# Performance work log

Measured on AMD Instinct MI355X. Metric: run time of the kernel, lower is better.

Reference implementation:

```python
import jax, jax.numpy as jnp
import numpy as np

S_GRID = 14.0
L_COORD = 5.0
L_NOOBJ = 0.5
B = 2


def _xywh2xyxy(b):
    # b: [..., 4] with (x, y, w, h); x,y are divided by S per the original module
    xy = b[..., :2] / S_GRID
    wh = b[..., 2:4]
    return jnp.concatenate([xy - 0.5 * wh, xy + 0.5 * wh], axis=-1)


def setup_inputs() -> dict:
    key = jax.random.key(0)
    k1, k2, k3, k4 = jax.random.split(key, 4)
    N, S, C = 4096, 14, 20
    pred_tensor = jax.random.uniform(k1, (N, S, S, B * 5 + C), dtype=jnp.float32, minval=0.05, maxval=1.0)
    target_boxes = jax.random.uniform(k2, (N, S, S, 4), dtype=jnp.float32, minval=0.05, maxval=1.0)
    target_cls = jax.random.normal(k3, (N, S, S, C), dtype=jnp.float32)
    has_object_map = jax.random.randint(k4, (N, S, S), 0, 2).astype(jnp.bool_)
    return {"pred_tensor": pred_tensor, "target_boxes": target_boxes,
            "target_cls": target_cls, "has_object_map": has_object_map}


def reference(pred_tensor, target_boxes, target_cls, has_object_map):
    N = pred_tensor.shape[0]
    mask = has_object_map                      # [N,S,S] bool
    maskf = mask.astype(pred_tensor.dtype)
    pb = pred_tensor[..., :B * 5].reshape(*pred_tensor.shape[:3], B, 5)  # [N,S,S,B,5]
    pc = pred_tensor[..., B * 5:]              # [N,S,S,20]

    # class loss: masked sum of squared errors over classes
    cls_loss = jnp.sum(maskf * jnp.sum((target_cls - pc) ** 2, axis=-1))

    # no-object loss: conf^2 on cells without objects, summed over both boxes
    conf = pb[..., 4]                          # [N,S,S,B]
    no_obj_loss = L_NOOBJ * jnp.sum(jnp.where(~mask[..., None], conf, 0.0) ** 2)

    # per-cell IoU of target vs each of the B predicted boxes (diag of original NxM)
    t_xyxy = _xywh2xyxy(target_boxes)          # [N,S,S,4]
    p_xyxy = _xywh2xyxy(pb[..., :4])           # [N,S,S,B,4]
    lt = jnp.maximum(t_xyxy[..., None, :2], p_xyxy[..., :2])
    rb = jnp.minimum(t_xyxy[..., None, 2:], p_xyxy[..., 2:])
    wh = jnp.clip(rb - lt, 0.0)
    inter = wh[..., 0] * wh[..., 1]            # [N,S,S,B]
    area_t = (t_xyxy[..., 2] - t_xyxy[..., 0]) * (t_xyxy[..., 3] - t_xyxy[..., 1])
    area_p = (p_xyxy[..., 2] - p_xyxy[..., 0]) * (p_xyxy[..., 3] - p_xyxy[..., 1])
    iou = inter / (area_t[..., None] + area_p - inter)  # [N,S,S,B]

    best_iou = jnp.max(iou, axis=-1)           # [N,S,S]
    best_idx = jnp.argmax(iou, axis=-1)        # [N,S,S]
    best_box = jnp.take_along_axis(pb, best_idx[..., None, None], axis=3)[..., 0, :]  # [N,S,S,5]

    xy_diff = jnp.where(mask[..., None], best_box[..., :2] - target_boxes[..., :2], 0.0)
    wh_p = jnp.where(mask[..., None], best_box[..., 2:4], 1.0)
    wh_t = jnp.where(mask[..., None], target_boxes[..., 2:4], 1.0)
    reg_loss = L_COORD * (jnp.sum(xy_diff ** 2)
                          + jnp.sum((jnp.sqrt(wh_p) - jnp.sqrt(wh_t)) ** 2))

    # containing-object confidence loss: mse(best_iou, best_box_conf) on object cells
    containing_obj_loss = jnp.sum(jnp.where(mask, best_iou - best_box[..., 4], 0.0) ** 2)

    total_loss = (cls_loss + no_obj_loss + reg_loss + containing_obj_loss) / N
    return (total_loss, reg_loss, containing_obj_loss, no_obj_loss, cls_loss)
```

## Files before the change

kernel.cpp:

```cpp
#include <hip/hip_runtime.h>
#include <math.h>


#define BLOCK 256
#define WPB 4
#define CPW 64

__global__ __launch_bounds__(BLOCK, 8) void k_yolo(
    const float*  __restrict__ pred,
    const float4* __restrict__ tbox4,
    const float2* __restrict__ tcls2,
    const int*    __restrict__ mask,
    float4*       __restrict__ partial,
    int n_cells)
{
    __shared__ float2 sbox[WPB][CPW * 5];
    const int tid  = threadIdx.x;
    const int lane = tid & 63;
    const int w    = tid >> 6;
    const long long cell0 = ((long long)blockIdx.x * WPB + w) * CPW;

    long long rem = (long long)n_cells - cell0;
    int lim = rem < 0 ? 0 : (rem > CPW ? CPW : (int)rem);

    float cls = 0.f, noobj = 0.f, reg = 0.f, cont = 0.f;

    int mflag = 0;
    float4 tb = make_float4(0.f, 0.f, 0.f, 0.f);
    if (lane < lim) {
        mflag = mask[cell0 + lane];
        tb    = tbox4[cell0 + lane];
    }

    const float2* p2  = reinterpret_cast<const float2*>(pred) + cell0 * 15;
    const float2* t2  = tcls2 + cell0 * 10;
    float2*       sb2 = sbox[w];

    #pragma unroll
    for (int k = 0; k < 15; ++k) {
        int j = lane + (k << 6);
        int c = j / 15;
        int r = j - c * 15;
        int mc = __shfl(mflag, c, 64);
        if (c < lim) {
            float2 v = p2[j];
            if (r < 5) {
                sb2[c * 5 + r] = v;
            } else if (mc) {
                float2 t = t2[c * 10 + (r - 5)];
                float d0 = t.x - v.x, d1 = t.y - v.y;
                cls = fmaf(d0, d0, cls);
                cls = fmaf(d1, d1, cls);
            }
        }
    }

    asm volatile("s_waitcnt lgkmcnt(0)" ::: "memory");
    __builtin_amdgcn_sched_barrier(0);

    if (lane < lim) {
        const float2* bl = sb2 + lane * 5;
        float2 v0 = bl[0], v1 = bl[1], v2 = bl[2], v3 = bl[3], v4 = bl[4];
        if (mflag) {
            float txc = tb.x / 14.0f, tyc = tb.y / 14.0f;
            float t0 = txc - 0.5f * tb.z, t1 = tyc - 0.5f * tb.w;
            float t2c = txc + 0.5f * tb.z, t3 = tyc + 0.5f * tb.w;
            float area_t = (t2c - t0) * (t3 - t1);
            float bx[2] = { v0.x, v2.y }, by[2] = { v0.y, v3.x };
            float bw[2] = { v1.x, v3.y }, bh[2] = { v1.y, v4.x };
            float bcf[2] = { v2.x, v4.y };
            float iou[2];
            #pragma unroll
            for (int b = 0; b < 2; ++b) {
                float px = bx[b] / 14.0f, py = by[b] / 14.0f;
                float q0 = px - 0.5f * bw[b], q1 = py - 0.5f * bh[b];
                float q2 = px + 0.5f * bw[b], q3 = py + 0.5f * bh[b];
                float lt0 = fmaxf(t0, q0), lt1 = fmaxf(t1, q1);
                float rb0 = fminf(t2c, q2), rb1 = fminf(t3, q3);
                float ww = fmaxf(rb0 - lt0, 0.f), hh = fmaxf(rb1 - lt1, 0.f);
                float inter = ww * hh;
                float area_p = (q2 - q0) * (q3 - q1);
                iou[b] = inter / (area_t + area_p - inter);
            }
            int bi = (iou[1] > iou[0]) ? 1 : 0;
            float dx = bx[bi] - tb.x, dy = by[bi] - tb.y;
            float swd = sqrtf(bw[bi]) - sqrtf(tb.z);
            float shd = sqrtf(bh[bi]) - sqrtf(tb.w);
            reg = 5.0f * (dx*dx + dy*dy + swd*swd + shd*shd);
            float dco = iou[bi] - bcf[bi];
            cont = dco * dco;
        } else {
            noobj = 0.5f * (v2.x * v2.x + v4.y * v4.y);
        }
    }

    #pragma unroll
    for (int off = 32; off; off >>= 1) {
        cls   += __shfl_down(cls,   off, 64);
        noobj += __shfl_down(noobj, off, 64);
        reg   += __shfl_down(reg,   off, 64);
        cont  += __shfl_down(cont,  off, 64);
    }
    __shared__ float4 swr[WPB];
    if (lane == 0) swr[w] = make_float4(cls, noobj, reg, cont);
    __syncthreads();
    if (tid == 0) {
        float4 a = swr[0];
        #pragma unroll
        for (int i = 1; i < WPB; ++i) {
            float4 b = swr[i];
            a.x += b.x; a.y += b.y; a.z += b.z; a.w += b.w;
        }
        partial[blockIdx.x] = a;
    }
}

__global__ __launch_bounds__(BLOCK) void k_final(
    const float4* __restrict__ partial, int nblocks,
    float* __restrict__ out, float invN)
{
    float4 acc = make_float4(0.f, 0.f, 0.f, 0.f);
    for (int b = threadIdx.x; b < nblocks; b += BLOCK) {
        float4 v = partial[b];
        acc.x += v.x; acc.y += v.y; acc.z += v.z; acc.w += v.w;
    }
    #pragma unroll
    for (int off = 32; off; off >>= 1) {
        acc.x += __shfl_down(acc.x, off, 64);
        acc.y += __shfl_down(acc.y, off, 64);
        acc.z += __shfl_down(acc.z, off, 64);
        acc.w += __shfl_down(acc.w, off, 64);
    }
    __shared__ float4 sw[WPB];
    int lane = threadIdx.x & 63, w = threadIdx.x >> 6;
    if (lane == 0) sw[w] = acc;
    __syncthreads();
    if (threadIdx.x == 0) {
        float cls = 0.f, noobj = 0.f, reg = 0.f, cont = 0.f;
        #pragma unroll
        for (int i = 0; i < WPB; ++i) {
            cls += sw[i].x; noobj += sw[i].y; reg += sw[i].z; cont += sw[i].w;
        }
        out[0] = (cls + noobj + reg + cont) * invN;
        out[1] = reg;
        out[2] = cont;
        out[3] = noobj;
        out[4] = cls;
    }
}

extern "C" void kernel_launch(void* const* d_in, const int* in_sizes, int n_in,
                              void* d_out, int out_size, void* d_ws, size_t ws_size,
                              hipStream_t stream) {
    const float*  pred  = (const float*)d_in[0];
    const float4* tbox4 = (const float4*)d_in[1];
    const float2* tcls2 = (const float2*)d_in[2];
    const int*    mask  = (const int*)d_in[3];
    float* out = (float*)d_out;
    float4* partial = (float4*)d_ws;

    int n_cells = in_sizes[3];
    int N = in_sizes[0] / (14 * 14 * 30);
    int nblocks = (n_cells + BLOCK - 1) / BLOCK;

    hipLaunchKernelGGL(k_yolo, dim3(nblocks), dim3(BLOCK), 0, stream,
                       pred, tbox4, tcls2, mask, partial, n_cells);
    hipLaunchKernelGGL(k_final, dim3(1), dim3(BLOCK), 0, stream,
                       partial, nblocks, out, 1.0f / (float)N);
}
```

Before: 207.3 us.

## Stage whole pred rows into LDS via global_load_lds and vectorize class loads

Each wave now copies its 64 cells of pred (30 floats each) straight from global memory into LDS with async global_load_lds 16-byte transfers, replacing the strided float2 gather loop with its divide-by-15 indexing. Each object-cell lane then reads its own target class row as five float4 loads and computes the class loss from LDS. This removes per-element index arithmetic and shuffles and widens the loads. The cost is a much larger LDS footprint (lower occupancy hint of 5), per-lane uncoalesced 80-byte tcls reads, and LDS bank conflicts from the 30-float row stride.

Result: faster. 200.2 us (-3.4%).

```diff
diff --git a/kernel.cpp b/kernel.cpp
--- a/kernel.cpp
+++ b/kernel.cpp
@@ -6,15 +6,15 @@
 #define WPB 4
 #define CPW 64
 
-__global__ __launch_bounds__(BLOCK, 8) void k_yolo(
+__global__ __launch_bounds__(BLOCK, 5) void k_yolo(
     const float*  __restrict__ pred,
     const float4* __restrict__ tbox4,
-    const float2* __restrict__ tcls2,
+    const float4* __restrict__ tcls4,
     const int*    __restrict__ mask,
     float4*       __restrict__ partial,
     int n_cells)
 {
-    __shared__ float2 sbox[WPB][CPW * 5];
+    __shared__ float sp[WPB][CPW * 30];
     const int tid  = threadIdx.x;
     const int lane = tid & 63;
     const int w    = tid >> 6;
@@ -32,35 +32,42 @@
         tb    = tbox4[cell0 + lane];
     }
 
-    const float2* p2  = reinterpret_cast<const float2*>(pred) + cell0 * 15;
-    const float2* t2  = tcls2 + cell0 * 10;
-    float2*       sb2 = sbox[w];
-
-    #pragma unroll
-    for (int k = 0; k < 15; ++k) {
-        int j = lane + (k << 6);
-        int c = j / 15;
-        int r = j - c * 15;
-        int mc = __shfl(mflag, c, 64);
-        if (c < lim) {
-            float2 v = p2[j];
-            if (r < 5) {
-                sb2[c * 5 + r] = v;
-            } else if (mc) {
-                float2 t = t2[c * 10 + (r - 5)];
-                float d0 = t.x - v.x, d1 = t.y - v.y;
-                cls = fmaf(d0, d0, cls);
-                cls = fmaf(d1, d1, cls);
-            }
+    if (lim == CPW) {
+        const __attribute__((address_space(1))) float4* gp =
+            (const __attribute__((address_space(1))) float4*)(pred + cell0 * 30);
+        __attribute__((address_space(3))) float4* lp =
+            (__attribute__((address_space(3))) float4*)(&sp[w][0]);
+        #pragma unroll
+        for (int i = 0; i < 7; ++i) {
+            __builtin_amdgcn_global_load_lds(
+                (const __attribute__((address_space(1))) void*)(gp + lane + i * 64),
+                (__attribute__((address_space(3))) void*)(lp + i * 64),
+                16, 0, 0);
         }
+        if (lane < 32) {
+            __builtin_amdgcn_global_load_lds(
+                (const __attribute__((address_space(1))) void*)(gp + 448 + lane),
+                (__attribute__((address_space(3))) void*)(lp + 448),
+                16, 0, 0);
+        }
+    } else if (lim > 0) {
+        const float* gsrc = pred + cell0 * 30;
+        for (int k = lane; k < lim * 30; k += 64) sp[w][k] = gsrc[k];
     }
 
-    asm volatile("s_waitcnt lgkmcnt(0)" ::: "memory");
+    float4 tc[5];
+    if (mflag) {
+        const float4* t4 = tcls4 + (cell0 + lane) * 5;
+        #pragma unroll
+        for (int q = 0; q < 5; ++q) tc[q] = t4[q];
+    }
+
+    asm volatile("s_waitcnt vmcnt(0) lgkmcnt(0)" ::: "memory");
     __builtin_amdgcn_sched_barrier(0);
 
     if (lane < lim) {
-        const float2* bl = sb2 + lane * 5;
-        float2 v0 = bl[0], v1 = bl[1], v2 = bl[2], v3 = bl[3], v4 = bl[4];
+        const float2* pc2 = reinterpret_cast<const float2*>(sp[w] + lane * 30);
+        float2 v0 = pc2[0], v1 = pc2[1], v2 = pc2[2], v3 = pc2[3], v4 = pc2[4];
         if (mflag) {
             float txc = tb.x / 14.0f, tyc = tb.y / 14.0f;
             float t0 = txc - 0.5f * tb.z, t1 = tyc - 0.5f * tb.w;
@@ -89,6 +96,18 @@
             reg = 5.0f * (dx*dx + dy*dy + swd*swd + shd*shd);
             float dco = iou[bi] - bcf[bi];
             cont = dco * dco;
+
+            #pragma unroll
+            for (int q = 0; q < 5; ++q) {
+                float2 a = pc2[5 + 2 * q];
+                float2 b = pc2[6 + 2 * q];
+                float d0 = tc[q].x - a.x, d1 = tc[q].y - a.y;
+                float d2 = tc[q].z - b.x, d3 = tc[q].w - b.y;
+                cls = fmaf(d0, d0, cls);
+                cls = fmaf(d1, d1, cls);
+                cls = fmaf(d2, d2, cls);
+                cls = fmaf(d3, d3, cls);
+            }
         } else {
             noobj = 0.5f * (v2.x * v2.x + v4.y * v4.y);
         }
@@ -154,7 +173,7 @@
                               hipStream_t stream) {
     const float*  pred  = (const float*)d_in[0];
     const float4* tbox4 = (const float4*)d_in[1];
-    const float2* tcls2 = (const float2*)d_in[2];
+    const float4* tcls4 = (const float4*)d_in[2];
     const int*    mask  = (const int*)d_in[3];
     float* out = (float*)d_out;
     float4* partial = (float4*)d_ws;
@@ -164,7 +183,7 @@
     int nblocks = (n_cells + BLOCK - 1) / BLOCK;
 
     hipLaunchKernelGGL(k_yolo, dim3(nblocks), dim3(BLOCK), 0, stream,
-                       pred, tbox4, tcls2, mask, partial, n_cells);
+                       pred, tbox4, tcls4, mask, partial, n_cells);
     hipLaunchKernelGGL(k_final, dim3(1), dim3(BLOCK), 0, stream,
                        partial, nblocks, out, 1.0f / (float)N);
 }
```

## Replace LDS-staged coalesced loads with per-thread direct cell loads

Applied to the files above, without the earlier changes.

The kernel stops staging prediction data through shared memory with wave-cooperative coalesced float2 loads and a cross-lane mask shuffle. Each thread now loads its own cell's 30 prediction floats and 20 target-class floats (as float4) straight into registers and computes all loss terms locally. This removes the LDS traffic, the shuffles and the index arithmetic, but the global loads become strided per thread (120-byte stride), which can hurt coalescing. Class targets are loaded even for cells without objects. Register pressure also rises, and the launch-bounds occupancy hint drops from 8 to 6.

After: 203.6 us. Within noise of the previous version (-1.8%).

```diff
diff --git a/kernel.cpp b/kernel.cpp
--- a/kernel.cpp
+++ b/kernel.cpp
@@ -4,63 +4,32 @@
 
 #define BLOCK 256
 #define WPB 4
-#define CPW 64
 
-__global__ __launch_bounds__(BLOCK, 8) void k_yolo(
+__global__ __launch_bounds__(BLOCK, 6) void k_yolo(
     const float*  __restrict__ pred,
     const float4* __restrict__ tbox4,
-    const float2* __restrict__ tcls2,
+    const float4* __restrict__ tcls4,
     const int*    __restrict__ mask,
     float4*       __restrict__ partial,
     int n_cells)
 {
-    __shared__ float2 sbox[WPB][CPW * 5];
     const int tid  = threadIdx.x;
-    const int lane = tid & 63;
-    const int w    = tid >> 6;
-    const long long cell0 = ((long long)blockIdx.x * WPB + w) * CPW;
-
-    long long rem = (long long)n_cells - cell0;
-    int lim = rem < 0 ? 0 : (rem > CPW ? CPW : (int)rem);
+    const int cell = blockIdx.x * BLOCK + tid;
+    const bool valid = cell < n_cells;
 
     float cls = 0.f, noobj = 0.f, reg = 0.f, cont = 0.f;
 
-    int mflag = 0;
-    float4 tb = make_float4(0.f, 0.f, 0.f, 0.f);
-    if (lane < lim) {
-        mflag = mask[cell0 + lane];
-        tb    = tbox4[cell0 + lane];
-    }
+    if (valid) {
+        const float2* pc2 = reinterpret_cast<const float2*>(pred + (size_t)cell * 30);
+        const float4* t4  = tcls4 + (size_t)cell * 5;
 
-    const float2* p2  = reinterpret_cast<const float2*>(pred) + cell0 * 15;
-    const float2* t2  = tcls2 + cell0 * 10;
-    float2*       sb2 = sbox[w];
+        const int    mflag = mask[cell];
+        const float4 tb    = tbox4[cell];
+        float2 v0  = pc2[0],  v1  = pc2[1],  v2  = pc2[2],  v3  = pc2[3],  v4  = pc2[4];
+        float2 v5  = pc2[5],  v6  = pc2[6],  v7  = pc2[7],  v8  = pc2[8],  v9  = pc2[9];
+        float2 v10 = pc2[10], v11 = pc2[11], v12 = pc2[12], v13 = pc2[13], v14 = pc2[14];
+        float4 tc0 = t4[0], tc1 = t4[1], tc2 = t4[2], tc3 = t4[3], tc4 = t4[4];
 
-    #pragma unroll
-    for (int k = 0; k < 15; ++k) {
-        int j = lane + (k << 6);
-        int c = j / 15;
-        int r = j - c * 15;
-        int mc = __shfl(mflag, c, 64);
-        if (c < lim) {
-            float2 v = p2[j];
-            if (r < 5) {
-                sb2[c * 5 + r] = v;
-            } else if (mc) {
-                float2 t = t2[c * 10 + (r - 5)];
-                float d0 = t.x - v.x, d1 = t.y - v.y;
-                cls = fmaf(d0, d0, cls);
-                cls = fmaf(d1, d1, cls);
-            }
-        }
-    }
-
-    asm volatile("s_waitcnt lgkmcnt(0)" ::: "memory");
-    __builtin_amdgcn_sched_barrier(0);
-
-    if (lane < lim) {
-        const float2* bl = sb2 + lane * 5;
-        float2 v0 = bl[0], v1 = bl[1], v2 = bl[2], v3 = bl[3], v4 = bl[4];
         if (mflag) {
             float txc = tb.x / 14.0f, tyc = tb.y / 14.0f;
             float t0 = txc - 0.5f * tb.z, t1 = tyc - 0.5f * tb.w;
@@ -89,6 +58,28 @@
             reg = 5.0f * (dx*dx + dy*dy + swd*swd + shd*shd);
             float dco = iou[bi] - bcf[bi];
             cont = dco * dco;
+
+            float d;
+            d = tc0.x - v5.x;  cls = fmaf(d, d, cls);
+            d = tc0.y - v5.y;  cls = fmaf(d, d, cls);
+            d = tc0.z - v6.x;  cls = fmaf(d, d, cls);
+            d = tc0.w - v6.y;  cls = fmaf(d, d, cls);
+            d = tc1.x - v7.x;  cls = fmaf(d, d, cls);
+            d = tc1.y - v7.y;  cls = fmaf(d, d, cls);
+            d = tc1.z - v8.x;  cls = fmaf(d, d, cls);
+            d = tc1.w - v8.y;  cls = fmaf(d, d, cls);
+            d = tc2.x - v9.x;  cls = fmaf(d, d, cls);
+            d = tc2.y - v9.y;  cls = fmaf(d, d, cls);
+            d = tc2.z - v10.x; cls = fmaf(d, d, cls);
+            d = tc2.w - v10.y; cls = fmaf(d, d, cls);
+            d = tc3.x - v11.x; cls = fmaf(d, d, cls);
+            d = tc3.y - v11.y; cls = fmaf(d, d, cls);
+            d = tc3.z - v12.x; cls = fmaf(d, d, cls);
+            d = tc3.w - v12.y; cls = fmaf(d, d, cls);
+            d = tc4.x - v13.x; cls = fmaf(d, d, cls);
+            d = tc4.y - v13.y; cls = fmaf(d, d, cls);
+            d = tc4.z - v14.x; cls = fmaf(d, d, cls);
+            d = tc4.w - v14.y; cls = fmaf(d, d, cls);
         } else {
             noobj = 0.5f * (v2.x * v2.x + v4.y * v4.y);
         }
@@ -102,6 +93,7 @@
         cont  += __shfl_down(cont,  off, 64);
     }
     __shared__ float4 swr[WPB];
+    const int lane = tid & 63, w = tid >> 6;
     if (lane == 0) swr[w] = make_float4(cls, noobj, reg, cont);
     __syncthreads();
     if (tid == 0) {
@@ -154,7 +146,7 @@
                               hipStream_t stream) {
     const float*  pred  = (const float*)d_in[0];
     const float4* tbox4 = (const float4*)d_in[1];
-    const float2* tcls2 = (const float2*)d_in[2];
+    const float4* tcls4 = (const float4*)d_in[2];
     const int*    mask  = (const int*)d_in[3];
     float* out = (float*)d_out;
     float4* partial = (float4*)d_ws;
@@ -164,7 +156,7 @@
     int nblocks = (n_cells + BLOCK - 1) / BLOCK;
 
     hipLaunchKernelGGL(k_yolo, dim3(nblocks), dim3(BLOCK), 0, stream,
-                       pred, tbox4, tcls2, mask, partial, n_cells);
+                       pred, tbox4, tcls4, mask, partial, n_cells);
     hipLaunchKernelGGL(k_final, dim3(1), dim3(BLOCK), 0, stream,
                        partial, nblocks, out, 1.0f / (float)N);
 }
```
